# Kernel tuning notes

Hardware: AMD Instinct MI355X
Metric: run time of the kernel (lower is better)

Reference implementation:

```python
import jax, jax.numpy as jnp
import numpy as np

B, M, N, K = 64, 1024, 1024, 128


def setup_inputs() -> dict:
    key = jax.random.key(0)
    k1, k2 = jax.random.split(key)
    # int8 operands in [-128, 127]; stored as int8 like the CUDA kernel expects
    a = jax.random.randint(k1, (B, M, K), -128, 128, dtype=jnp.int32).astype(jnp.int8)
    b = jax.random.randint(k2, (B, N, K), -128, 128, dtype=jnp.int32).astype(jnp.int8)
    # alpha = a_scale * b_scale / output_scale (scalar buffer 'a' in the module)
    alpha = jnp.float32(0.0078125)
    return {"a": a, "b": b, "alpha": alpha}


def reference(a, b, alpha):
    acc = jnp.einsum("bmk,bnk->bmn", a.astype(jnp.int32), b.astype(jnp.int32))  # [B,M,N] int32
    # fused epilogue: scale by alpha, round-to-nearest, store as int32 (s32t output)
    return jnp.round(acc.astype(jnp.float32) * alpha).astype(jnp.int32)
```

## Files before the change

### kernel.cpp

```cpp
#include <hip/hip_runtime.h>
#include <stdint.h>


typedef int v4i  __attribute__((ext_vector_type(4)));
typedef int v16i __attribute__((ext_vector_type(16)));

__device__ __forceinline__ int pack4(v4i w) {
    return (w.x & 0xFF) | ((w.y & 0xFF) << 8) | ((w.z & 0xFF) << 16) | (w.w << 24);
}

__global__ __launch_bounds__(256, 4) void bmm_s8s8_s32_kernel(
    const int*   __restrict__ A,
    const int*   __restrict__ Bm,
    const float* __restrict__ alpha_p,
    int*         __restrict__ out)
{
    __shared__ uint8_t smem[32768];
    uint8_t* Als   = smem;
    uint8_t* Bls   = smem + 16384;
    int*     chunk = (int*)smem;

    const int tid   = threadIdx.x;
    const int lane  = tid & 63;
    const int wave  = tid >> 6;
    const int half_ = lane >> 5;
    const int lrow  = lane & 31;

    const int bz = blockIdx.z;
    const int m0 = blockIdx.y << 7;
    const int n0 = blockIdx.x << 7;

    const float alpha = *alpha_p;

    const size_t abase = ((size_t)bz * 1024 + (size_t)m0) * 128;
    const size_t bbase = ((size_t)bz * 1024 + (size_t)n0) * 128;

#pragma unroll
    for (int t = 0; t < 4; ++t) {
        const int G  = t * 256 + tid;
        const int m  = G >> 3;
        const int gp = G & 7;
        const size_t goff = (size_t)m * 128 + (size_t)gp * 16;

        v4i a0 = *(const v4i*)(A + abase + goff + 0);
        v4i a1 = *(const v4i*)(A + abase + goff + 4);
        v4i a2 = *(const v4i*)(A + abase + goff + 8);
        v4i a3 = *(const v4i*)(A + abase + goff + 12);
        v4i b0 = *(const v4i*)(Bm + bbase + goff + 0);
        v4i b1 = *(const v4i*)(Bm + bbase + goff + 4);
        v4i b2 = *(const v4i*)(Bm + bbase + goff + 8);
        v4i b3 = *(const v4i*)(Bm + bbase + goff + 12);

        v4i pa = { pack4(a0), pack4(a1), pack4(a2), pack4(a3) };
        v4i pb = { pack4(b0), pack4(b1), pack4(b2), pack4(b3) };

        const int loff = m * 128 + ((gp ^ (m & 7)) << 4);
        *(v4i*)(Als + loff) = pa;
        *(v4i*)(Bls + loff) = pb;
    }
    __syncthreads();

    v16i acc[4] = {};

#pragma unroll
    for (int kk = 0; kk < 4; ++kk) {
        const int g = kk * 2 + half_;
        const int n = wave * 32 + lrow;
        const v4i bf = *(const v4i*)(Bls + n * 128 + ((g ^ (n & 7)) << 4));
        v4i af[4];
#pragma unroll
        for (int mi = 0; mi < 4; ++mi) {
            const int m = mi * 32 + lrow;
            af[mi] = *(const v4i*)(Als + m * 128 + ((g ^ (m & 7)) << 4));
        }
#pragma unroll
        for (int mi = 0; mi < 4; ++mi)
            acc[mi] = __builtin_amdgcn_mfma_i32_32x32x32_i8(af[mi], bf, acc[mi], 0, 0, 0);
    }
    __syncthreads();

    int* outb = out + ((size_t)bz << 20) + n0;

#pragma unroll
    for (int j = 0; j < 4; ++j) {
#pragma unroll
        for (int r = 0; r < 16; ++r) {
            const int row_local = (r & 3) + 8 * (r >> 2) + 4 * half_;
            chunk[row_local * 128 + wave * 32 + lrow] =
                __float2int_rn((float)acc[j][r] * alpha);
        }
        __syncthreads();
#pragma unroll
        for (int p = 0; p < 4; ++p) {
            const int row_local = p * 8 + (tid >> 5);
            const v4i v = *(const v4i*)((const uint8_t*)chunk + p * 4096 + tid * 16);
            *(v4i*)(outb + (size_t)(m0 + j * 32 + row_local) * 1024 + (tid & 31) * 4) = v;
        }
        if (j < 3) __syncthreads();
    }
}

extern "C" void kernel_launch(void* const* d_in, const int* in_sizes, int n_in,
                              void* d_out, int out_size, void* d_ws, size_t ws_size,
                              hipStream_t stream) {
    const int*   A     = (const int*)d_in[0];
    const int*   Bm    = (const int*)d_in[1];
    const float* alpha = (const float*)d_in[2];
    int*         out   = (int*)d_out;

    dim3 grid(8, 8, 64);
    dim3 block(256);
    bmm_s8s8_s32_kernel<<<grid, block, 0, stream>>>(A, Bm, alpha, out);
}
```

Measured before the change: 350.7 us.

## Prepack int32 operands to int8 in a separate pass and stream output stores

Adds a prepass kernel that packs the int32-stored A and B operands into dense int8 buffers in the workspace. The GEMM kernel then loads a quarter of the bytes for each tile, which matters because each tile is reread by several blocks. Output writes become nontemporal stores. The cost is an extra kernel launch plus one full read of the inputs and a workspace write.

```diff
diff --git a/kernel.cpp b/kernel.cpp
--- a/kernel.cpp
+++ b/kernel.cpp
@@ -9,11 +9,30 @@
     return (w.x & 0xFF) | ((w.y & 0xFF) << 8) | ((w.z & 0xFF) << 16) | (w.w << 24);
 }
 
+__global__ __launch_bounds__(256) void prepack_kernel(
+    const int* __restrict__ A, const int* __restrict__ Bm,
+    uint8_t* __restrict__ Apk, uint8_t* __restrict__ Bpk)
+{
+    const int g = blockIdx.x * 256 + threadIdx.x;
+    const size_t eoff = (size_t)g * 16;
+
+    v4i a[4], b[4];
+#pragma unroll
+    for (int i = 0; i < 4; ++i) {
+        a[i] = __builtin_nontemporal_load((const v4i*)(A + eoff) + i);
+        b[i] = __builtin_nontemporal_load((const v4i*)(Bm + eoff) + i);
+    }
+    v4i pa = { pack4(a[0]), pack4(a[1]), pack4(a[2]), pack4(a[3]) };
+    v4i pb = { pack4(b[0]), pack4(b[1]), pack4(b[2]), pack4(b[3]) };
+    *(v4i*)(Apk + eoff) = pa;
+    *(v4i*)(Bpk + eoff) = pb;
+}
+
 __global__ __launch_bounds__(256, 4) void bmm_s8s8_s32_kernel(
-    const int*   __restrict__ A,
-    const int*   __restrict__ Bm,
-    const float* __restrict__ alpha_p,
-    int*         __restrict__ out)
+    const uint8_t* __restrict__ Apk,
+    const uint8_t* __restrict__ Bpk,
+    const float*   __restrict__ alpha_p,
+    int*           __restrict__ out)
 {
     __shared__ uint8_t smem[32768];
     uint8_t* Als   = smem;
@@ -40,20 +59,8 @@
         const int G  = t * 256 + tid;
         const int m  = G >> 3;
         const int gp = G & 7;
-        const size_t goff = (size_t)m * 128 + (size_t)gp * 16;
-
-        v4i a0 = *(const v4i*)(A + abase + goff + 0);
-        v4i a1 = *(const v4i*)(A + abase + goff + 4);
-        v4i a2 = *(const v4i*)(A + abase + goff + 8);
-        v4i a3 = *(const v4i*)(A + abase + goff + 12);
-        v4i b0 = *(const v4i*)(Bm + bbase + goff + 0);
-        v4i b1 = *(const v4i*)(Bm + bbase + goff + 4);
-        v4i b2 = *(const v4i*)(Bm + bbase + goff + 8);
-        v4i b3 = *(const v4i*)(Bm + bbase + goff + 12);
-
-        v4i pa = { pack4(a0), pack4(a1), pack4(a2), pack4(a3) };
-        v4i pb = { pack4(b0), pack4(b1), pack4(b2), pack4(b3) };
-
+        const v4i pa = *(const v4i*)(Apk + abase + (size_t)G * 16);
+        const v4i pb = *(const v4i*)(Bpk + bbase + (size_t)G * 16);
         const int loff = m * 128 + ((gp ^ (m & 7)) << 4);
         *(v4i*)(Als + loff) = pa;
         *(v4i*)(Bls + loff) = pb;
@@ -61,7 +68,6 @@
     __syncthreads();
 
     v16i acc[4] = {};
-
 #pragma unroll
     for (int kk = 0; kk < 4; ++kk) {
         const int g = kk * 2 + half_;
@@ -94,7 +100,8 @@
         for (int p = 0; p < 4; ++p) {
             const int row_local = p * 8 + (tid >> 5);
             const v4i v = *(const v4i*)((const uint8_t*)chunk + p * 4096 + tid * 16);
-            *(v4i*)(outb + (size_t)(m0 + j * 32 + row_local) * 1024 + (tid & 31) * 4) = v;
+            __builtin_nontemporal_store(
+                v, (v4i*)(outb + (size_t)(m0 + j * 32 + row_local) * 1024 + (tid & 31) * 4));
         }
         if (j < 3) __syncthreads();
     }
@@ -108,7 +115,11 @@
     const float* alpha = (const float*)d_in[2];
     int*         out   = (int*)d_out;
 
+    uint8_t* Apk = (uint8_t*)d_ws;
+    uint8_t* Bpk = (uint8_t*)d_ws + (8u << 20);
+
+    prepack_kernel<<<dim3(2048), dim3(256), 0, stream>>>(A, Bm, Apk, Bpk);
+
     dim3 grid(8, 8, 64);
-    dim3 block(256);
-    bmm_s8s8_s32_kernel<<<grid, block, 0, stream>>>(A, Bm, alpha, out);
+    bmm_s8s8_s32_kernel<<<grid, dim3(256), 0, stream>>>(Apk, Bpk, alpha, out);
 }
```

Measured after the change: 323.0 us. 1.09x faster.
